# Kernel tuning notes

Hardware: AMD Instinct MI355X
Metric: run time of the kernel (lower is better)

The kernel has to match this reference:

```python
import jax, jax.numpy as jnp
import numpy as np

B, CLIP, P, E, H = 1024, 1024, 32, 2048, 16  # batch, clip_dim, prefix_length, token_emb_dim, num_heads
DH = E // H  # head dim = 128


def setup_inputs() -> dict:
    key = jax.random.key(0)
    ks = jax.random.split(key, 8)
    w = lambda k, sh: (jax.random.normal(k, sh, jnp.float32) * 0.02)
    return {
        "image_embs": jax.random.normal(ks[0], (B, CLIP), jnp.float32),
        "Wm": w(ks[1], (E, CLIP)),           # memory_proj weight
        "bm": jnp.zeros((E,), jnp.float32),
        "prefix_queries": w(ks[2], (P, E)),   # learned prefix queries
        "Win": w(ks[3], (3 * E, E)),          # MHA packed in_proj weight [q;k;v]
        "bin": jnp.zeros((3 * E,), jnp.float32),
        "Wo_mha": w(ks[4], (E, E)),           # MHA out_proj
        "bo_mha": jnp.zeros((E,), jnp.float32),
        "Wo": w(ks[5], (E, E)),               # adapter out_proj
        "bo": jnp.zeros((E,), jnp.float32),
    }


def reference(image_embs, Wm, bm, prefix_queries, Win, bin, Wo_mha, bo_mha, Wo, bo):
    Bn = image_embs.shape[0]
    # memory_proj: (B, clip_dim) -> (B, E); memory seq length is 1
    mem = image_embs @ Wm.T + bm
    # packed q/k/v projections, as in nn.MultiheadAttention
    Wq, Wk, Wv = Win[:E], Win[E:2 * E], Win[2 * E:]
    bq, bk, bv = bin[:E], bin[E:2 * E], bin[2 * E:]
    q = prefix_queries @ Wq.T + bq          # (P, E), shared across batch (queries are expanded)
    k = mem @ Wk.T + bk                     # (B, E)
    v = mem @ Wv.T + bv                     # (B, E)
    qh = q.reshape(P, H, DH)                # (P, H, dh)
    kh = k.reshape(Bn, H, DH)               # (B, H, dh)
    vh = v.reshape(Bn, H, DH)               # (B, H, dh)
    # scaled dot-product attention with kv_len = 1
    scores = jnp.einsum("phd,bhd->bhp", qh, kh) / jnp.sqrt(jnp.float32(DH))  # (B, H, P)
    attn = jax.nn.softmax(scores[..., None], axis=-1)  # (B, H, P, 1); trivially all-ones
    attn_out = jnp.einsum("bhpk,bhkd->bphd", attn, vh[:, :, None, :])  # (B, P, H, dh)
    attn_out = attn_out.reshape(Bn, P, E)
    out = attn_out @ Wo_mha.T + bo_mha      # MHA out_proj
    out = out @ Wo.T + bo                   # adapter out_proj
    return out
```

## Files before the change

### kernel.cpp

```cpp
#include <hip/hip_runtime.h>


#define BM 128
#define BN 64
#define BK 64
#define NBUF 4

typedef __attribute__((ext_vector_type(8))) __bf16 bf16x8;
typedef __attribute__((ext_vector_type(4))) float f32x4;

__device__ __forceinline__ unsigned short f2bf(float f) {
  unsigned int u = __float_as_uint(f);
  u += 0x7FFFu + ((u >> 16) & 1u);
  return (unsigned short)(u >> 16);
}

__device__ __forceinline__ void gload_lds16(const void* g, void* l) {
  __builtin_amdgcn_global_load_lds(
      (const __attribute__((address_space(1))) void*)g,
      (__attribute__((address_space(3))) void*)l, 16, 0, 0);
}

__global__ __launch_bounds__(256) void cvt_xw(const float* __restrict__ x,
                                              const float* __restrict__ wm,
                                              unsigned short* __restrict__ dst) {
  size_t i = (size_t)blockIdx.x * blockDim.x + threadIdx.x;
  for (; i < 786432; i += 262144) {
    const float4 v = (i < 262144)
        ? reinterpret_cast<const float4*>(x)[i]
        : reinterpret_cast<const float4*>(wm)[i - 262144];
    ushort4 o;
    o.x = f2bf(v.x); o.y = f2bf(v.y); o.z = f2bf(v.z); o.w = f2bf(v.w);
    reinterpret_cast<ushort4*>(dst)[i] = o;
  }
}

template <int EPI, bool CVT>
__global__ __launch_bounds__(512, 1) void gemm_bt(
    const unsigned short* __restrict__ A, const unsigned short* __restrict__ W,
    const float* __restrict__ bias, void* __restrict__ outp, int K,
    const float* __restrict__ cvt_src, unsigned short* __restrict__ cvt_dst,
    int cvt_n4) {
  __shared__ __attribute__((aligned(16))) unsigned short As[NBUF][BM * BK];
  __shared__ __attribute__((aligned(16))) unsigned short Bs[NBUF][BN * BK];
  const int tid = threadIdx.x;
  const int lane = tid & 63;
  const int wid = tid >> 6;
  const int rm = (wid >> 1) * 32;
  const int cn = (wid & 1) * 32;
  const int bid = blockIdx.x;
  const int bn0 = ((bid & 7) * 4 + (bid >> 6)) * BN;
  const int bm0 = ((bid >> 3) & 7) * BM;
  const int l15 = lane & 15;
  const int l4 = lane >> 4;
  const int lr = lane >> 3;
  const int lc = lane & 7;
  const int scol = ((lc ^ lr) << 3);
  const size_t Kz = (size_t)K;

  f32x4 acc[2][2] = {};

  auto stage = [&](int buf, int tile) {
    const int k0 = tile * BK;
#pragma unroll
    for (int j = 0; j < 2; ++j) {
      const int c = wid * 2 + j;
      gload_lds16(A + (size_t)(bm0 + c * 8 + lr) * Kz + (k0 + scol),
                  &As[buf][c * 512]);
    }
    gload_lds16(W + (size_t)(bn0 + wid * 8 + lr) * Kz + (k0 + scol),
                &Bs[buf][wid * 512]);
  };

  auto compute = [&](int buf) {
    const int swz = (l15 & 7) << 3;
#pragma unroll
    for (int ks = 0; ks < 2; ++ks) {
      const int kidx = (ks * 32 + l4 * 8) ^ swz;
      bf16x8 a[2], b[2];
#pragma unroll
      for (int mi = 0; mi < 2; ++mi)
        a[mi] = *reinterpret_cast<const bf16x8*>(
            &As[buf][(rm + mi * 16 + l15) * 64 + kidx]);
#pragma unroll
      for (int ni = 0; ni < 2; ++ni)
        b[ni] = *reinterpret_cast<const bf16x8*>(
            &Bs[buf][(cn + ni * 16 + l15) * 64 + kidx]);
#pragma unroll
      for (int mi = 0; mi < 2; ++mi)
#pragma unroll
        for (int ni = 0; ni < 2; ++ni)
          acc[mi][ni] = __builtin_amdgcn_mfma_f32_16x16x32_bf16(
              a[mi], b[ni], acc[mi][ni], 0, 0, 0);
    }
  };

  const int nt = K >> 6;
  stage(0, 0); stage(1, 1); stage(2, 2);
  int t = 0;
  for (; t < nt - 3; ++t) {
    asm volatile("s_waitcnt vmcnt(6)" ::: "memory");
    asm volatile("s_waitcnt lgkmcnt(0)" ::: "memory");
    __builtin_amdgcn_s_barrier();
    stage((t + 3) & 3, t + 3);
    compute(t & 3);
  }
  asm volatile("s_waitcnt vmcnt(6) lgkmcnt(0)" ::: "memory");
  __builtin_amdgcn_s_barrier();
  compute(t & 3); ++t;
  asm volatile("s_waitcnt vmcnt(3) lgkmcnt(0)" ::: "memory");
  __builtin_amdgcn_s_barrier();
  compute(t & 3); ++t;
  asm volatile("s_waitcnt vmcnt(0) lgkmcnt(0)" ::: "memory");
  __builtin_amdgcn_s_barrier();
  compute(t & 3);

  if (EPI == 0) {
#pragma unroll
    for (int mi = 0; mi < 2; ++mi)
#pragma unroll
      for (int ni = 0; ni < 2; ++ni) {
        const int col = bn0 + cn + ni * 16 + l15;
        const float bcol = bias[col];
#pragma unroll
        for (int i = 0; i < 4; ++i) {
          const int row = bm0 + rm + mi * 16 + l4 * 4 + i;
          ((unsigned short*)outp)[(size_t)row * 2048 + col] =
              f2bf(acc[mi][ni][i] + bcol);
        }
      }
  } else {
    asm volatile("s_waitcnt lgkmcnt(0)" ::: "memory");
    __builtin_amdgcn_s_barrier();
    float* Cs = (float*)As;
#pragma unroll
    for (int mi = 0; mi < 2; ++mi)
#pragma unroll
      for (int ni = 0; ni < 2; ++ni) {
        const int col = cn + ni * 16 + l15;
        const float bcol = bias[bn0 + col];
#pragma unroll
        for (int i = 0; i < 4; ++i)
          Cs[(rm + mi * 16 + l4 * 4 + i) * 68 + col] = acc[mi][ni][i] + bcol;
      }
    asm volatile("s_waitcnt lgkmcnt(0)" ::: "memory");
    __builtin_amdgcn_s_barrier();
    float* out = (float*)outp;
    const int c4 = (lane & 15) * 4;
#pragma unroll
    for (int it = 0; it < 4; ++it) {
      const int rl = wid * 16 + it * 4 + (lane >> 4);
      const f32x4 v = *reinterpret_cast<const f32x4*>(&Cs[rl * 68 + c4]);
      float* ob = out + ((size_t)(bm0 + rl) * 32) * 2048 + bn0 + c4;
#pragma unroll 8
      for (int p = 0; p < 32; ++p)
        __builtin_nontemporal_store(v, reinterpret_cast<f32x4*>(ob + p * 2048));
    }
  }

  if (CVT) {
    size_t i = (size_t)bid * 512 + tid;
    for (; i < (size_t)cvt_n4; i += 131072) {
      const float4 v = reinterpret_cast<const float4*>(cvt_src)[i];
      ushort4 o;
      o.x = f2bf(v.x); o.y = f2bf(v.y); o.z = f2bf(v.z); o.w = f2bf(v.w);
      reinterpret_cast<ushort4*>(cvt_dst)[i] = o;
    }
  }
}

extern "C" void kernel_launch(void* const* d_in, const int* in_sizes, int n_in,
                              void* d_out, int out_size, void* d_ws, size_t ws_size,
                              hipStream_t stream) {
  const float* image = (const float*)d_in[0];
  const float* Wm   = (const float*)d_in[1];
  const float* bm   = (const float*)d_in[2];
  const float* Win  = (const float*)d_in[4];
  const float* bin  = (const float*)d_in[5];
  const float* Wo1  = (const float*)d_in[6];
  const float* bo1  = (const float*)d_in[7];
  const float* Wo2  = (const float*)d_in[8];
  const float* bo2  = (const float*)d_in[9];
  float* out = (float*)d_out;

  const float* Wv = Win + (size_t)2 * 2048 * 2048;
  const float* bv = bin + 2 * 2048;

  unsigned short* wsb = (unsigned short*)d_ws;
  unsigned short* Xb   = wsb;
  unsigned short* Wmb  = wsb + (1u << 20);
  unsigned short* Wvb  = wsb + (3u << 20);
  unsigned short* W1b  = wsb + (7u << 20);
  unsigned short* W2b  = wsb + (11u << 20);
  unsigned short* act0 = wsb + (15u << 20);
  unsigned short* act1 = wsb + (17u << 20);
  unsigned short* act2 = wsb + (19u << 20);

  cvt_xw<<<1024, 256, 0, stream>>>(image, Wm, wsb);

  gemm_bt<0, true><<<256, 512, 0, stream>>>(Xb, Wmb, bm, act0, 1024,
                                            Wv, Wvb, 1048576);
  gemm_bt<0, true><<<256, 512, 0, stream>>>(act0, Wvb, bv, act1, 2048,
                                            Wo1, W1b, 1048576);
  gemm_bt<0, true><<<256, 512, 0, stream>>>(act1, W1b, bo1, act2, 2048,
                                            Wo2, W2b, 1048576);
  gemm_bt<1, false><<<256, 512, 0, stream>>>(act2, W2b, bo2, out, 2048,
                                             nullptr, nullptr, 0);
  (void)n_in; (void)in_sizes; (void)out_size; (void)ws_size;
}
```

Measured before the change: 155.3 us.

## Load GEMM B operand directly into registers and unroll K loop at compile time

The weight (B) tile is no longer staged through LDS with global_load_lds; each wave loads its bf16x8 B fragments straight from global memory into a 4-slot register ring two tiles ahead. The K extent becomes a template parameter, so the main loop is fully unrolled and the vmcnt waits are chosen per iteration. This is meant to remove the LDS write/read traffic and ds_read latency for B. In exchange, the four waves that share a column block fetch the same B rows redundantly through cache, and register pressure rises.

```diff
diff --git a/kernel.cpp b/kernel.cpp
--- a/kernel.cpp
+++ b/kernel.cpp
@@ -35,14 +35,13 @@
   }
 }
 
-template <int EPI, bool CVT>
+template <int NT, int EPI, bool CVT>
 __global__ __launch_bounds__(512, 1) void gemm_bt(
     const unsigned short* __restrict__ A, const unsigned short* __restrict__ W,
-    const float* __restrict__ bias, void* __restrict__ outp, int K,
+    const float* __restrict__ bias, void* __restrict__ outp,
     const float* __restrict__ cvt_src, unsigned short* __restrict__ cvt_dst,
     int cvt_n4) {
   __shared__ __attribute__((aligned(16))) unsigned short As[NBUF][BM * BK];
-  __shared__ __attribute__((aligned(16))) unsigned short Bs[NBUF][BN * BK];
   const int tid = threadIdx.x;
   const int lane = tid & 63;
   const int wid = tid >> 6;
@@ -56,11 +55,12 @@
   const int lr = lane >> 3;
   const int lc = lane & 7;
   const int scol = ((lc ^ lr) << 3);
-  const size_t Kz = (size_t)K;
+  const size_t Kz = (size_t)(NT * 64);
 
   f32x4 acc[2][2] = {};
-
-  auto stage = [&](int buf, int tile) {
+  bf16x8 breg[NBUF][2][2];
+
+  auto stageA = [&](int buf, int tile) {
     const int k0 = tile * BK;
 #pragma unroll
     for (int j = 0; j < 2; ++j) {
@@ -68,52 +68,54 @@
       gload_lds16(A + (size_t)(bm0 + c * 8 + lr) * Kz + (k0 + scol),
                   &As[buf][c * 512]);
     }
-    gload_lds16(W + (size_t)(bn0 + wid * 8 + lr) * Kz + (k0 + scol),
-                &Bs[buf][wid * 512]);
   };
 
-  auto compute = [&](int buf) {
+  auto loadB = [&](int slot, int tile) {
+    const int k0 = tile * BK;
+#pragma unroll
+    for (int ni = 0; ni < 2; ++ni)
+#pragma unroll
+      for (int ks = 0; ks < 2; ++ks)
+        breg[slot][ni][ks] = *reinterpret_cast<const bf16x8*>(
+            W + (size_t)(bn0 + cn + ni * 16 + l15) * Kz + (k0 + ks * 32 + l4 * 8));
+  };
+
+  auto compute = [&](int buf, int slot) {
     const int swz = (l15 & 7) << 3;
 #pragma unroll
     for (int ks = 0; ks < 2; ++ks) {
       const int kidx = (ks * 32 + l4 * 8) ^ swz;
-      bf16x8 a[2], b[2];
+      bf16x8 a[2];
 #pragma unroll
       for (int mi = 0; mi < 2; ++mi)
         a[mi] = *reinterpret_cast<const bf16x8*>(
             &As[buf][(rm + mi * 16 + l15) * 64 + kidx]);
 #pragma unroll
-      for (int ni = 0; ni < 2; ++ni)
-        b[ni] = *reinterpret_cast<const bf16x8*>(
-            &Bs[buf][(cn + ni * 16 + l15) * 64 + kidx]);
-#pragma unroll
       for (int mi = 0; mi < 2; ++mi)
 #pragma unroll
         for (int ni = 0; ni < 2; ++ni)
           acc[mi][ni] = __builtin_amdgcn_mfma_f32_16x16x32_bf16(
-              a[mi], b[ni], acc[mi][ni], 0, 0, 0);
+              a[mi], breg[slot][ni][ks], acc[mi][ni], 0, 0, 0);
     }
   };
 
-  const int nt = K >> 6;
-  stage(0, 0); stage(1, 1); stage(2, 2);
-  int t = 0;
-  for (; t < nt - 3; ++t) {
-    asm volatile("s_waitcnt vmcnt(6)" ::: "memory");
+  stageA(0, 0); stageA(1, 1); loadB(0, 0); stageA(2, 2); loadB(1, 1);
+#pragma unroll
+  for (int t = 0; t < NT; ++t) {
+    if (t + 3 < NT) stageA((t + 3) & 3, t + 3);
+    if (t + 2 < NT) loadB((t + 2) & 3, t + 2);
+    if (t < NT - 3)
+      asm volatile("s_waitcnt vmcnt(12)" ::: "memory");
+    else if (t == NT - 3)
+      asm volatile("s_waitcnt vmcnt(10)" ::: "memory");
+    else if (t == NT - 2)
+      asm volatile("s_waitcnt vmcnt(4)" ::: "memory");
+    else
+      asm volatile("s_waitcnt vmcnt(0)" ::: "memory");
     asm volatile("s_waitcnt lgkmcnt(0)" ::: "memory");
     __builtin_amdgcn_s_barrier();
-    stage((t + 3) & 3, t + 3);
-    compute(t & 3);
-  }
-  asm volatile("s_waitcnt vmcnt(6) lgkmcnt(0)" ::: "memory");
-  __builtin_amdgcn_s_barrier();
-  compute(t & 3); ++t;
-  asm volatile("s_waitcnt vmcnt(3) lgkmcnt(0)" ::: "memory");
-  __builtin_amdgcn_s_barrier();
-  compute(t & 3); ++t;
-  asm volatile("s_waitcnt vmcnt(0) lgkmcnt(0)" ::: "memory");
-  __builtin_amdgcn_s_barrier();
-  compute(t & 3);
+    compute(t & 3, t & 3);
+  }
 
   if (EPI == 0) {
 #pragma unroll
@@ -198,13 +200,13 @@
 
   cvt_xw<<<1024, 256, 0, stream>>>(image, Wm, wsb);
 
-  gemm_bt<0, true><<<256, 512, 0, stream>>>(Xb, Wmb, bm, act0, 1024,
-                                            Wv, Wvb, 1048576);
-  gemm_bt<0, true><<<256, 512, 0, stream>>>(act0, Wvb, bv, act1, 2048,
-                                            Wo1, W1b, 1048576);
-  gemm_bt<0, true><<<256, 512, 0, stream>>>(act1, W1b, bo1, act2, 2048,
-                                            Wo2, W2b, 1048576);
-  gemm_bt<1, false><<<256, 512, 0, stream>>>(act2, W2b, bo2, out, 2048,
-                                             nullptr, nullptr, 0);
+  gemm_bt<16, 0, true><<<256, 512, 0, stream>>>(Xb, Wmb, bm, act0,
+                                                Wv, Wvb, 1048576);
+  gemm_bt<32, 0, true><<<256, 512, 0, stream>>>(act0, Wvb, bv, act1,
+                                                Wo1, W1b, 1048576);
+  gemm_bt<32, 0, true><<<256, 512, 0, stream>>>(act1, W1b, bo1, act2,
+                                                Wo2, W2b, 1048576);
+  gemm_bt<32, 1, false><<<256, 512, 0, stream>>>(act2, W2b, bo2, out,
+                                                 nullptr, nullptr, 0);
   (void)n_in; (void)in_sizes; (void)out_size; (void)ws_size;
 }
```

New measurement: 194.7 us. 1.25x slower.
